# Kernel tuning notes

Hardware: AMD Instinct MI355X
Metric: run time of the kernel (lower is better)

The kernel has to match this reference:

```python
import jax, jax.numpy as jnp
import numpy as np

N, E = 16384, 262144
NS_N, NV_N = 128, 64      # node irreps: 128x0e + 64x1o
NS_E, NV_E = 64, 32       # edge irreps: 64x0e + 32x1o
C_OH, LAT = 16, 128
DS, DV = 128, 64          # irreps_out: 128x0e + 64x1o
GS = DS + DV              # gate input scalars (128 act scalars + 64 gates)
SC = 2 * NS_N + NS_E      # 320 concatenated scalar channels
VC = 2 * NV_N + NV_E      # 160 concatenated l=1 channels
M0_IN = SC + VC           # 480 m=0 features into SO2 linear
M0_OUT = GS + DV          # 256 m=0 outputs
AVG_NEI = 16.0
EPS = 1e-8


def setup_inputs() -> dict:
    key = jax.random.key(0)
    ks = jax.random.split(key, 20)
    f = lambda k, s: jax.random.normal(k, s, dtype=jnp.float32)
    return dict(
        node_feat=f(ks[0], (N, NS_N + 3 * NV_N)),
        edge_feat=f(ks[1], (E, NS_E + 3 * NV_E)),
        edge_vec=f(ks[2], (E, 3)),
        latents=f(ks[3], (E, LAT)),
        node_onehot=jax.nn.one_hot(jax.random.randint(ks[4], (N,), 0, C_OH), C_OH, dtype=jnp.float32),
        ln_n_g0=jnp.ones(NS_N), ln_n_b0=jnp.zeros(NS_N), ln_n_g1=jnp.ones(NV_N),
        ln_e_g0=jnp.ones(NS_E), ln_e_b0=jnp.zeros(NS_E), ln_e_g1=jnp.ones(NV_E),
        W_m0=f(ks[5], (M0_IN, M0_OUT)),
        w_r=f(ks[6], (VC, DV)), w_i=f(ks[7], (VC, DV)),
        W_env=f(ks[8], (LAT, DS + DV)),
        Wp0=f(ks[9], (DS, DS)), bp0=jnp.zeros(DS), Wpv=f(ks[10], (DV, DV)),
        Wtp0=f(ks[11], (DS, C_OH, GS)), Wtp1=f(ks[12], (DV, C_OH, DV)),
        Wo0=f(ks[13], (DS, DS)), bo0=jnp.zeros(DS), Wov=f(ks[14], (DV, DV)),
        res_param=jnp.zeros(()),
        edge_index=jax.random.randint(ks[15], (2, E), 0, N),
    )


def _sep_ln(s, v, g0, b0, g1):
    # separable equivariant layer norm: LN on scalars, per-sample RMS on l=1 block
    mu = s.mean(-1, keepdims=True)
    var = jnp.mean((s - mu) ** 2, -1, keepdims=True)
    s = (s - mu) * jax.lax.rsqrt(var + EPS) * g0 + b0
    vvar = jnp.mean(v * v, axis=(-2, -1), keepdims=True)  # component norm, degree-balanced (single l=1)
    v = v * jax.lax.rsqrt(vvar + EPS) * g1[None, :, None]
    return s, v


def _edge_frame(vec):
    # orthonormal frame (a, e1, e2) with a along the edge
    a = vec * jax.lax.rsqrt(jnp.sum(vec * vec, -1, keepdims=True) + EPS)
    helper = jnp.where(jnp.abs(a[:, 2:3]) < 0.99,
                       jnp.array([0.0, 0.0, 1.0], dtype=vec.dtype),
                       jnp.array([1.0, 0.0, 0.0], dtype=vec.dtype))
    e1 = jnp.cross(helper, a)
    e1 = e1 * jax.lax.rsqrt(jnp.sum(e1 * e1, -1, keepdims=True) + EPS)
    e2 = jnp.cross(a, e1)
    return a, e1, e2


def reference(node_feat, edge_feat, edge_vec, latents, node_onehot,
              ln_n_g0, ln_n_b0, ln_n_g1, ln_e_g0, ln_e_b0, ln_e_g1,
              W_m0, w_r, w_i, W_env, Wp0, bp0, Wpv,
              Wtp0, Wtp1, Wo0, bo0, Wov, res_param, edge_index):
    src, dst = edge_index[0], edge_index[1]
    ns, nv = node_feat[:, :NS_N], node_feat[:, NS_N:].reshape(-1, NV_N, 3)
    es, ev = edge_feat[:, :NS_E], edge_feat[:, NS_E:].reshape(-1, NV_E, 3)
    ns, nv = _sep_ln(ns, nv, ln_n_g0, ln_n_b0, ln_n_g1)
    es, ev = _sep_ln(es, ev, ln_e_g0, ln_e_b0, ln_e_g1)
    # per-edge concat: node[src] + edge + node[dst]
    s_cat = jnp.concatenate([ns[src], es, ns[dst]], -1)          # [E, SC]
    v_cat = jnp.concatenate([nv[src], ev, nv[dst]], 1)           # [E, VC, 3]
    # SO2 linear: rotate into edge frame, mix per |m|, rotate back
    a, e1, e2 = _edge_frame(edge_vec)
    c0 = jnp.einsum('eci,ei->ec', v_cat, a)
    c1 = jnp.einsum('eci,ei->ec', v_cat, e1)
    c2 = jnp.einsum('eci,ei->ec', v_cat, e2)
    m0 = jnp.concatenate([s_cat, c0], -1) @ W_m0 * (1.0 / np.sqrt(M0_IN))  # [E, M0_OUT]
    s_out, c0o = m0[:, :GS], m0[:, GS:]
    inv = 1.0 / np.sqrt(VC)
    c1o = (c1 @ w_r - c2 @ w_i) * inv
    c2o = (c1 @ w_i + c2 @ w_r) * inv
    v_out = (c0o[..., None] * a[:, None, :] + c1o[..., None] * e1[:, None, :]
             + c2o[..., None] * e2[:, None, :])                  # [E, DV, 3]
    # gate activation
    s_act = jax.nn.silu(s_out[:, :DS])
    gates = jax.nn.sigmoid(s_out[:, DS:])
    v_g = v_out * gates[..., None]
    # lin_post (per-l linear, scalar bias)
    s2 = s_act @ Wp0 * (1.0 / np.sqrt(DS)) + bp0
    v2 = jnp.einsum('eui,uv->evi', v_g, Wpv) * (1.0 / np.sqrt(DV))
    # env weighting from latents (E3ElementLinear, per-irrep-channel scalars)
    w = latents @ W_env * (1.0 / np.sqrt(LAT))
    s2 = s2 * w[:, :DS]
    v2 = v2 * w[:, DS:, None]
    nrm = 1.0 / np.sqrt(AVG_NEI)
    sa = jax.ops.segment_sum(s2, dst, num_segments=N) * nrm
    va = jax.ops.segment_sum(v2, dst, num_segments=N) * nrm
    # one-hot FullyConnectedTensorProduct (in2 all 0e) + gate + linear
    t0 = jnp.einsum('nu,nc,ucv->nv', sa, node_onehot, Wtp0) * (1.0 / np.sqrt(DS * C_OH))
    t1 = jnp.einsum('nui,nc,ucv->nvi', va, node_onehot, Wtp1) * (1.0 / np.sqrt(DV * C_OH))
    s3 = jax.nn.silu(t0[:, :DS])
    v3 = t1 * jax.nn.sigmoid(t0[:, DS:])[..., None]
    s4 = s3 @ Wo0 * (1.0 / np.sqrt(DS)) + bo0
    v4 = jnp.einsum('nui,uv->nvi', v3, Wov) * (1.0 / np.sqrt(DV))
    new = jnp.concatenate([s4, v4.reshape(-1, 3 * DV)], -1)
    r = jax.nn.sigmoid(res_param)
    return r * node_feat + (1.0 - r) * new
```

## Files before the change

### kernel.cpp

```cpp
#include <hip/hip_runtime.h>
#include <math.h>

#define N_NODES 16384
#define N_EDGES 262144
#define EPSF 1e-8f

#define OFF_X     0
#define OFF_C12   31232
#define OFF_FR    52224
#define OFF_EDST  53760
#define POOL_BYTES 53888
#define OFF_SACT  0
#define OFF_GATE  8704
#define OFF_C0O   17408
#define OFF_C1O   31232
#define OFF_C2O   39936
#define OFF_VG    8704

typedef __bf16 bf16x8 __attribute__((ext_vector_type(8)));
typedef float  f32x4  __attribute__((ext_vector_type(4)));

__device__ __forceinline__ f32x4 MFMA16(bf16x8 a, bf16x8 b, f32x4 c){
  return __builtin_amdgcn_mfma_f32_16x16x32_bf16(a, b, c, 0, 0, 0);
}

__device__ __forceinline__ unsigned short f2bf(float x){
  union { float f; unsigned u; } c; c.f = x;
  unsigned u = c.u;
  u += 0x7FFFu + ((u>>16)&1u);
  return (unsigned short)(u>>16);
}
__device__ __forceinline__ float bf2f(unsigned short h){
  union { unsigned u; float f; } c; c.u = ((unsigned)h)<<16;
  return c.f;
}
__device__ __forceinline__ float wsum64(float v){
  #pragma unroll
  for (int m=1; m<64; m<<=1) v += __shfl_xor(v, m);
  return v;
}
__device__ __forceinline__ float wsum32(float v){
  #pragma unroll
  for (int m=1; m<32; m<<=1) v += __shfl_xor(v, m);
  return v;
}
__device__ __forceinline__ float sigm(float x){ return 1.0f/(1.0f+__expf(-x)); }
__device__ __forceinline__ float silu(float x){ return x/(1.0f+__expf(-x)); }

__global__ __launch_bounds__(256) void k_pack(const float* __restrict__ src,
                                              unsigned short* __restrict__ dst,
                                              int K, int N){
  int i = blockIdx.x*256 + threadIdx.x;
  if (i >= K*N) return;
  int k = i / N, n = i - k*N;
  int idx = (((k>>5)*N + n)*4 + ((k>>3)&3))*8 + (k&7);
  dst[idx] = f2bf(src[i]);
}
__global__ __launch_bounds__(256) void k_pack_wc(const float* __restrict__ wr,
                                                 const float* __restrict__ wi,
                                                 unsigned short* __restrict__ dst){
  int i = blockIdx.x*256 + threadIdx.x;
  if (i >= 320*128) return;
  int k = i >> 7, n = i & 127;
  float v;
  if (k < 160) v = (n < 64) ? wr[k*64 + n]        : wi[k*64 + (n-64)];
  else         v = (n < 64) ? -wi[(k-160)*64 + n] : wr[(k-160)*64 + (n-64)];
  int idx = (((k>>5)*128 + n)*4 + ((k>>3)&3))*8 + (k&7);
  dst[idx] = f2bf(v);
}

__global__ __launch_bounds__(256) void k_hist(const int* __restrict__ eidx, int* __restrict__ cnt){
  int e = blockIdx.x*256 + threadIdx.x;
  if (e < N_EDGES) atomicAdd(&cnt[eidx[N_EDGES+e]], 1);
}
__global__ __launch_bounds__(256) void k_scan(const int* __restrict__ cnt,
                                              int* __restrict__ rowp, int* __restrict__ cursor){
  __shared__ int part[256];
  __shared__ int pref[257];
  const int t = threadIdx.x;
  const int base = t*64;
  int s = 0;
  for (int i=0;i<64;i++) s += cnt[base+i];
  part[t] = s; __syncthreads();
  if (t==0){ int a=0; for (int i=0;i<256;i++){ pref[i]=a; a+=part[i]; } pref[256]=a; }
  __syncthreads();
  int a = pref[t];
  for (int i=0;i<64;i++){ rowp[base+i]=a; cursor[base+i]=a; a += cnt[base+i]; }
  if (t==0) rowp[N_NODES] = pref[256];
}
__global__ __launch_bounds__(256) void k_fill(const int* __restrict__ eidx,
                                              int* __restrict__ cursor, int* __restrict__ perm){
  int e = blockIdx.x*256 + threadIdx.x;
  if (e < N_EDGES){
    int pos = atomicAdd(&cursor[eidx[N_EDGES+e]], 1);
    perm[pos] = e;
  }
}

__global__ __launch_bounds__(256) void k_node_ln(
    const float* __restrict__ nf, const float* __restrict__ g0,
    const float* __restrict__ b0, const float* __restrict__ g1,
    unsigned short* __restrict__ ns_ln, float* __restrict__ nv_ln)
{
  const int tid  = threadIdx.x;
  const int lane = tid & 63;
  const int n    = blockIdx.x*4 + (tid>>6);
  const float* row = nf + (size_t)n*320;

  float s0 = row[lane], s1 = row[64+lane];
  float mu = wsum64(s0+s1) * (1.0f/128.0f);
  float d0 = s0-mu, d1 = s1-mu;
  float var = wsum64(d0*d0+d1*d1) * (1.0f/128.0f);
  float rs = rsqrtf(var + EPSF);
  ns_ln[(size_t)n*128 + lane]    = f2bf(d0*rs*g0[lane]    + b0[lane]);
  ns_ln[(size_t)n*128 + 64+lane] = f2bf(d1*rs*g0[64+lane] + b0[64+lane]);

  float px = row[128+lane*3+0], py = row[128+lane*3+1], pz = row[128+lane*3+2];
  float vvar = wsum64(px*px+py*py+pz*pz) * (1.0f/192.0f);
  float vsc = rsqrtf(vvar + EPSF) * g1[lane];
  nv_ln[(size_t)n*192 + lane*3+0] = px*vsc;
  nv_ln[(size_t)n*192 + lane*3+1] = py*vsc;
  nv_ln[(size_t)n*192 + lane*3+2] = pz*vsc;
}

__global__ __launch_bounds__(256) void k_wenv(
  const float* __restrict__ lats, const unsigned short* __restrict__ pWenv,
  const int* __restrict__ perm, unsigned short* __restrict__ wbuf)
{
  __shared__ unsigned short A[64*136];
  const int tid = threadIdx.x;
  {
    const int row = tid>>2, part = tid&3;
    const int slot = blockIdx.x*64 + row;
    const int e = perm[slot];
    const float* lr = lats + (size_t)e*128 + part*32;
    #pragma unroll
    for (int q=0;q<8;q++){
      float4 v = *(const float4*)(lr + q*4);
      int cb = part*32 + q*4;
      A[row*136 + cb+0] = f2bf(v.x);
      A[row*136 + cb+1] = f2bf(v.y);
      A[row*136 + cb+2] = f2bf(v.z);
      A[row*136 + cb+3] = f2bf(v.w);
    }
  }
  __syncthreads();
  const int wid = tid>>6, l = tid&63, r15 = l&15, g = l>>4;
  const f32x4 zero4 = {0.f,0.f,0.f,0.f};
  f32x4 acc[4][3];
  #pragma unroll
  for (int m=0;m<4;m++)
    #pragma unroll
    for (int n=0;n<3;n++) acc[m][n]=zero4;

  const unsigned short* bbase = pWenv + ((size_t)(wid*48 + r15)*4 + g)*8;
  #pragma unroll
  for (int kc=0;kc<4;kc++){
    bf16x8 b[3];
    #pragma unroll
    for (int n=0;n<3;n++) b[n] = *(const bf16x8*)(bbase + (size_t)kc*6144 + n*512);
    #pragma unroll
    for (int m=0;m<4;m++){
      bf16x8 a = *(const bf16x8*)&A[(m*16+r15)*136 + kc*32 + g*8];
      #pragma unroll
      for (int n=0;n<3;n++) acc[m][n] = MFMA16(a, b[n], acc[m][n]);
    }
  }
  #pragma unroll
  for (int m=0;m<4;m++)
    #pragma unroll
    for (int n=0;n<3;n++)
      #pragma unroll
      for (int r=0;r<4;r++){
        int sr = m*16 + g*4 + r;
        int j  = wid*48 + n*16 + r15;
        wbuf[(size_t)(blockIdx.x*64 + sr)*192 + j] = f2bf(acc[m][n][r]*0.08838834764831845f);
      }
}

__global__ __launch_bounds__(256,3) void k_edge(
  const float* __restrict__ ef, const float* __restrict__ evec,
  const float* __restrict__ g0e, const float* __restrict__ b0e, const float* __restrict__ g1e,
  const unsigned short* __restrict__ pWm0, const unsigned short* __restrict__ pWc,
  const unsigned short* __restrict__ pWp0, const unsigned short* __restrict__ pWpv,
  const float* __restrict__ bp0,
  const int* __restrict__ eidx, const int* __restrict__ perm,
  const unsigned short* __restrict__ ns_ln, const float* __restrict__ nv_ln,
  const unsigned short* __restrict__ wbuf,
  float* __restrict__ sa, float* __restrict__ va)
{
  extern __shared__ unsigned char pool[];
  const int tid = threadIdx.x;
  unsigned short* Xs   = (unsigned short*)(pool + OFF_X);
  unsigned short* C12s = (unsigned short*)(pool + OFF_C12);
  float* FRf = (float*)(pool + OFF_FR);
  int*   EDST = (int*)(pool + OFF_EDST);

  {
    const int ln = tid & 31;
    #pragma unroll
    for (int eo=0; eo<4; ++eo){
      const int el = eo*8 + (tid>>5);
      const int slot = blockIdx.x*32 + el;
      const size_t e = (size_t)perm[slot];
      const int src = eidx[e];
      const int dst = eidx[N_EDGES + e];

      float vx=evec[e*3+0], vy=evec[e*3+1], vz=evec[e*3+2];
      float rn = rsqrtf(vx*vx+vy*vy+vz*vz+EPSF);
      float ax=vx*rn, ay=vy*rn, az=vz*rn;
      float hx, hz;
      if (fabsf(az) < 0.99f){ hx=0.f; hz=1.f; } else { hx=1.f; hz=0.f; }
      float e1x = -hz*ay;
      float e1y = hz*ax - hx*az;
      float e1z = hx*ay;
      float rn1 = rsqrtf(e1x*e1x+e1y*e1y+e1z*e1z+EPSF);
      e1x*=rn1; e1y*=rn1; e1z*=rn1;
      float e2x = ay*e1z - az*e1y;
      float e2y = az*e1x - ax*e1z;
      float e2z = ax*e1y - ay*e1x;
      if (ln==0){
        FRf[el*12+0]=ax;  FRf[el*12+1]=ay;  FRf[el*12+2]=az;
        FRf[el*12+3]=e1x; FRf[el*12+4]=e1y; FRf[el*12+5]=e1z;
        FRf[el*12+6]=e2x; FRf[el*12+7]=e2y; FRf[el*12+8]=e2z;
        EDST[el]=dst;
      }

      const float* erow = ef + e*160;
      float s0=erow[ln], s1=erow[32+ln];
      float mu = wsum32(s0+s1)*(1.f/64.f);
      float d0=s0-mu, d1=s1-mu;
      float var = wsum32(d0*d0+d1*d1)*(1.f/64.f);
      float rs = rsqrtf(var+EPSF);
      Xs[el*488 + 128+ln] = f2bf(d0*rs*g0e[ln]    + b0e[ln]);
      Xs[el*488 + 160+ln] = f2bf(d1*rs*g0e[32+ln] + b0e[32+ln]);

      float wx=erow[64+ln*3+0], wy=erow[64+ln*3+1], wz=erow[64+ln*3+2];
      float vvar = wsum32(wx*wx+wy*wy+wz*wz)*(1.f/96.f);
      float vsc = rsqrtf(vvar+EPSF)*g1e[ln];
      wx*=vsc; wy*=vsc; wz*=vsc;
      Xs  [el*488 + 320+64+ln]   = f2bf(wx*ax +wy*ay +wz*az);
      C12s[el*328 + 64+ln]       = f2bf(wx*e1x+wy*e1y+wz*e1z);
      C12s[el*328 + 160+64+ln]   = f2bf(wx*e2x+wy*e2y+wz*e2z);

      const unsigned short* nss = ns_ln + (size_t)src*128;
      const unsigned short* nsd = ns_ln + (size_t)dst*128;
      *(uint2*)&Xs[el*488 + ln*4]       = *(const uint2*)&nss[ln*4];
      *(uint2*)&Xs[el*488 + 192 + ln*4] = *(const uint2*)&nsd[ln*4];

      const float* nvs = nv_ln + (size_t)src*192;
      const float* nvd = nv_ln + (size_t)dst*192;
      #pragma unroll
      for (int q=0;q<2;q++){
        int u = ln+32*q;
        float px=nvs[u*3+0], py=nvs[u*3+1], pz=nvs[u*3+2];
        Xs  [el*488 + 320+u]     = f2bf(px*ax +py*ay +pz*az);
        C12s[el*328 + u]         = f2bf(px*e1x+py*e1y+pz*e1z);
        C12s[el*328 + 160+u]     = f2bf(px*e2x+py*e2y+pz*e2z);
        px=nvd[u*3+0]; py=nvd[u*3+1]; pz=nvd[u*3+2];
        Xs  [el*488 + 320+96+u]  = f2bf(px*ax +py*ay +pz*az);
        C12s[el*328 + 96+u]      = f2bf(px*e1x+py*e1y+pz*e1z);
        C12s[el*328 + 160+96+u]  = f2bf(px*e2x+py*e2y+pz*e2z);
      }
    }
  }
  __syncthreads();

  const int wid = tid>>6, l = tid&63;
  const int r15 = l&15, g = l>>4;
  const f32x4 zero4 = {0.f,0.f,0.f,0.f};

  f32x4 acc1[2][4], acc2[2][2];
  #pragma unroll
  for (int m=0;m<2;m++){
    #pragma unroll
    for (int n=0;n<4;n++) acc1[m][n]=zero4;
    #pragma unroll
    for (int n=0;n<2;n++) acc2[m][n]=zero4;
  }

  {
    const unsigned short* bbase = pWm0 + ((size_t)(wid*64 + r15)*4 + g)*8;
    bf16x8 bc[4];
    #pragma unroll
    for (int n=0;n<4;n++) bc[n] = *(const bf16x8*)(bbase + n*512);
    for (int kc=0;kc<15;kc++){
      bf16x8 a0 = *(const bf16x8*)&Xs[(    r15)*488 + kc*32 + g*8];
      bf16x8 a1 = *(const bf16x8*)&Xs[(16+ r15)*488 + kc*32 + g*8];
      bf16x8 bn[4];
      if (kc<14){
        const unsigned short* np = bbase + (size_t)(kc+1)*8192;
        #pragma unroll
        for (int n=0;n<4;n++) bn[n] = *(const bf16x8*)(np + n*512);
      }
      #pragma unroll
      for (int n=0;n<4;n++){
        acc1[0][n] = MFMA16(a0,bc[n],acc1[0][n]);
        acc1[1][n] = MFMA16(a1,bc[n],acc1[1][n]);
      }
      #pragma unroll
      for (int n=0;n<4;n++) bc[n]=bn[n];
    }
  }
  {
    const unsigned short* bbase = pWc + ((size_t)(wid*32 + r15)*4 + g)*8;
    bf16x8 bc[2];
    #pragma unroll
    for (int n=0;n<2;n++) bc[n] = *(const bf16x8*)(bbase + n*512);
    for (int kc=0;kc<10;kc++){
      bf16x8 a0 = *(const bf16x8*)&C12s[(    r15)*328 + kc*32 + g*8];
      bf16x8 a1 = *(const bf16x8*)&C12s[(16+ r15)*328 + kc*32 + g*8];
      bf16x8 bn[2];
      if (kc<9){
        const unsigned short* np = bbase + (size_t)(kc+1)*4096;
        #pragma unroll
        for (int n=0;n<2;n++) bn[n] = *(const bf16x8*)(np + n*512);
      }
      #pragma unroll
      for (int n=0;n<2;n++){
        acc2[0][n] = MFMA16(a0,bc[n],acc2[0][n]);
        acc2[1][n] = MFMA16(a1,bc[n],acc2[1][n]);
      }
      #pragma unroll
      for (int n=0;n<2;n++) bc[n]=bn[n];
    }
  }

  __syncthreads();

  {
    unsigned short* SAs = (unsigned short*)(pool + OFF_SACT);
    float* GAf = (float*)(pool + OFF_GATE);
    float* C0f = (float*)(pool + OFF_C0O);
    #pragma unroll
    for (int m=0;m<2;m++)
      #pragma unroll
      for (int n=0;n<4;n++)
        #pragma unroll
        for (int r=0;r<4;r++){
          int e = m*16 + g*4 + r;
          int j = wid*64 + n*16 + r15;
          float v = acc1[m][n][r]*0.04564354645876384f;
          if (j < 128)      SAs[e*136 + j] = f2bf(silu(v));
          else if (j < 192) GAf[e*68 + (j-128)] = sigm(v);
          else              C0f[e*68 + (j-192)] = v;
        }
    float* C1f = (float*)(pool + OFF_C1O);
    float* C2f = (float*)(pool + OFF_C2O);
    #pragma unroll
    for (int m=0;m<2;m++)
      #pragma unroll
      for (int n=0;n<2;n++)
        #pragma unroll
        for (int r=0;r<4;r++){
          int e = m*16 + g*4 + r;
          int j = wid*32 + n*16 + r15;
          float v = acc2[m][n][r]*0.07905694150420949f;
          if (j < 64) C1f[e*68 + j] = v;
          else        C2f[e*68 + (j-64)] = v;
        }
  }
  __syncthreads();

  {
    const int e = tid>>3, u0 = (tid&7)*8;
    const float* GAf = (const float*)(pool + OFF_GATE);
    const float* C0f = (const float*)(pool + OFF_C0O);
    const float* C1f = (const float*)(pool + OFF_C1O);
    const float* C2f = (const float*)(pool + OFF_C2O);
    float ax=FRf[e*12+0],  ay=FRf[e*12+1],  az=FRf[e*12+2];
    float b1x=FRf[e*12+3], b1y=FRf[e*12+4], b1z=FRf[e*12+5];
    float b2x=FRf[e*12+6], b2y=FRf[e*12+7], b2z=FRf[e*12+8];
    float vgx[8], vgy[8], vgz[8];
    #pragma unroll
    for (int i=0;i<8;i++){
      int u = u0+i;
      float gt = GAf[e*68+u];
      float c0 = C0f[e*68+u], c1 = C1f[e*68+u], c2 = C2f[e*68+u];
      vgx[i] = (c0*ax + c1*b1x + c2*b2x)*gt;
      vgy[i] = (c0*ay + c1*b1y + c2*b2y)*gt;
      vgz[i] = (c0*az + c1*b1z + c2*b2z)*gt;
    }
    __syncthreads();
    unsigned short* VGs = (unsigned short*)(pool + OFF_VG);
    #pragma unroll
    for (int i=0;i<8;i++){
      VGs[0*2304 + e*72 + u0+i] = f2bf(vgx[i]);
      VGs[1*2304 + e*72 + u0+i] = f2bf(vgy[i]);
      VGs[2*2304 + e*72 + u0+i] = f2bf(vgz[i]);
    }
  }
  __syncthreads();

  {
    const unsigned short* SAs = (const unsigned short*)(pool + OFF_SACT);
    const unsigned short* VGs = (const unsigned short*)(pool + OFF_VG);
    const int sbase = blockIdx.x*32;

    float wsc[2][2][4], wvc[2][4], bp0v[2];
    #pragma unroll
    for (int n=0;n<2;n++) bp0v[n] = bp0[wid*32 + n*16 + r15];
    #pragma unroll
    for (int m=0;m<2;m++)
      #pragma unroll
      for (int r=0;r<4;r++){
        int e = m*16 + g*4 + r;
        #pragma unroll
        for (int n=0;n<2;n++)
          wsc[m][n][r] = bf2f(wbuf[(size_t)(sbase+e)*192 + wid*32 + n*16 + r15]);
        wvc[m][r] = bf2f(wbuf[(size_t)(sbase+e)*192 + 128 + wid*16 + r15]);
      }

    f32x4 acc4[2][2], acc5[3][2];
    #pragma unroll
    for (int m=0;m<2;m++){ acc4[m][0]=zero4; acc4[m][1]=zero4; }
    #pragma unroll
    for (int c=0;c<3;c++){ acc5[c][0]=zero4; acc5[c][1]=zero4; }

    {
      const unsigned short* bbase = pWp0 + ((size_t)(wid*32 + r15)*4 + g)*8;
      #pragma unroll
      for (int kc=0;kc<4;kc++){
        bf16x8 a0 = *(const bf16x8*)&SAs[(    r15)*136 + kc*32 + g*8];
        bf16x8 a1 = *(const bf16x8*)&SAs[(16+ r15)*136 + kc*32 + g*8];
        #pragma unroll
        for (int n=0;n<2;n++){
          bf16x8 b = *(const bf16x8*)(bbase + (size_t)kc*4096 + n*512);
          acc4[0][n] = MFMA16(a0,b,acc4[0][n]);
          acc4[1][n] = MFMA16(a1,b,acc4[1][n]);
        }
      }
    }
    {
      bf16x8 b5[2];
      #pragma unroll
      for (int kc=0;kc<2;kc++)
        b5[kc] = *(const bf16x8*)(pWpv + ((size_t)(kc*64 + wid*16 + r15)*4 + g)*8);
      #pragma unroll
      for (int c=0;c<3;c++)
        #pragma unroll
        for (int kc=0;kc<2;kc++){
          bf16x8 a0 = *(const bf16x8*)&VGs[c*2304 + (    r15)*72 + kc*32 + g*8];
          bf16x8 a1 = *(const bf16x8*)&VGs[c*2304 + (16+ r15)*72 + kc*32 + g*8];
          acc5[c][0] = MFMA16(a0,b5[kc],acc5[c][0]);
          acc5[c][1] = MFMA16(a1,b5[kc],acc5[c][1]);
        }
    }

    __syncthreads();
    float* R = (float*)pool;
    #pragma unroll
    for (int m=0;m<2;m++)
      #pragma unroll
      for (int n=0;n<2;n++)
        #pragma unroll
        for (int r=0;r<4;r++){
          int e = m*16 + g*4 + r;
          int j = wid*32 + n*16 + r15;
          R[e*320 + j] = (acc4[m][n][r]*0.08838834764831845f + bp0v[n]) * wsc[m][n][r];
        }
    #pragma unroll
    for (int c=0;c<3;c++)
      #pragma unroll
      for (int m=0;m<2;m++)
        #pragma unroll
        for (int r=0;r<4;r++){
          int e = m*16 + g*4 + r;
          int vch = wid*16 + r15;
          R[e*320 + 128 + vch*3 + c] = acc5[c][m][r]*0.125f * wvc[m][r];
        }
    __syncthreads();

    for (int j = tid; j < 320; j += 256){
      float accv = R[j];
      int cur = EDST[0];
      for (int e=1;e<32;e++){
        int d = EDST[e];
        float v = R[e*320 + j];
        if (d != cur){
          float* tgt = (j<128) ? &sa[(size_t)cur*128 + j] : &va[(size_t)cur*192 + (j-128)];
          atomicAdd(tgt, accv);
          accv = v; cur = d;
        } else accv += v;
      }
      float* tgt = (j<128) ? &sa[(size_t)cur*128 + j] : &va[(size_t)cur*192 + (j-128)];
      atomicAdd(tgt, accv);
    }
  }
}

__global__ __launch_bounds__(256) void k_node_out(
  const float* __restrict__ nf, const float* __restrict__ oh,
  const float* __restrict__ Wtp0, const float* __restrict__ Wtp1,
  const float* __restrict__ Wo0, const float* __restrict__ bo0,
  const float* __restrict__ Wov, const float* __restrict__ resp,
  const float* __restrict__ sa, const float* __restrict__ va,
  float* __restrict__ out)
{
  __shared__ float SAB[4][128];
  __shared__ float VX[4][64], VY[4][64], VZ[4][64];
  __shared__ float S3 [4][128];
  __shared__ float V3 [4][256];
  const int tid=threadIdx.x, lane=tid&63, g=tid>>6;
  const int n = blockIdx.x*4 + g;

  float cf=0.f;
  #pragma unroll
  for (int j=0;j<16;j++) cf += j*oh[(size_t)n*16+j];
  const int c = (int)(cf+0.5f);

  SAB[g][lane]    = sa[(size_t)n*128+lane]   *0.25f;
  SAB[g][64+lane] = sa[(size_t)n*128+64+lane]*0.25f;
  VX[g][lane] = va[(size_t)n*192+lane*3+0]*0.25f;
  VY[g][lane] = va[(size_t)n*192+lane*3+1]*0.25f;
  VZ[g][lane] = va[(size_t)n*192+lane*3+2]*0.25f;
  __syncthreads();

  float t00=0.f, t01=0.f, t02=0.f;
  const float* w0c = Wtp0 + (size_t)c*192;
  for (int u=0;u<128;u++){
    float s = SAB[g][u];
    t00 += s * w0c[(size_t)u*3072 + lane];
    t01 += s * w0c[(size_t)u*3072 + lane+64];
    t02 += s * w0c[(size_t)u*3072 + lane+128];
  }
  const float sct0 = 0.02209708691f;
  t00*=sct0; t01*=sct0; t02*=sct0;

  float t1x=0.f,t1y=0.f,t1z=0.f;
  const float* w1c = Wtp1 + (size_t)c*64;
  for (int u=0;u<64;u++){
    float wv = w1c[(size_t)u*1024 + lane];
    t1x += VX[g][u]*wv;
    t1y += VY[g][u]*wv;
    t1z += VZ[g][u]*wv;
  }
  t1x*=0.03125f; t1y*=0.03125f; t1z*=0.03125f;

  S3[g][lane]    = silu(t00);
  S3[g][64+lane] = silu(t01);
  float g2 = sigm(t02);
  float4 v3v = {t1x*g2, t1y*g2, t1z*g2, 0.f};
  *(float4*)&V3[g][lane*4] = v3v;
  __syncthreads();

  float s40=0.f, s41=0.f;
  for (int k=0;k<128;k++){
    float s3k = S3[g][k];
    s40 += s3k*Wo0[k*128+lane];
    s41 += s3k*Wo0[k*128+64+lane];
  }
  s40 = s40*0.08838834765f + bo0[lane];
  s41 = s41*0.08838834765f + bo0[64+lane];

  float v4x=0.f,v4y=0.f,v4z=0.f;
  for (int u=0;u<64;u++){
    float4 v3u = *(const float4*)&V3[g][u*4];
    float wv = Wov[u*64+lane];
    v4x += v3u.x*wv; v4y += v3u.y*wv; v4z += v3u.z*wv;
  }
  v4x*=0.125f; v4y*=0.125f; v4z*=0.125f;

  const float r = sigm(resp[0]);
  const float* row = nf + (size_t)n*320;
  float* orow = out + (size_t)n*320;
  orow[lane]      = r*row[lane]      + (1.f-r)*s40;
  orow[64+lane]   = r*row[64+lane]   + (1.f-r)*s41;
  orow[128+lane*3+0] = r*row[128+lane*3+0] + (1.f-r)*v4x;
  orow[128+lane*3+1] = r*row[128+lane*3+1] + (1.f-r)*v4y;
  orow[128+lane*3+2] = r*row[128+lane*3+2] + (1.f-r)*v4z;
}

extern "C" void kernel_launch(void* const* d_in, const int* in_sizes, int n_in,
                              void* d_out, int out_size, void* d_ws, size_t ws_size,
                              hipStream_t stream)
{
  const float* nf   = (const float*)d_in[0];
  const float* ef   = (const float*)d_in[1];
  const float* evec = (const float*)d_in[2];
  const float* lats = (const float*)d_in[3];
  const float* oh   = (const float*)d_in[4];
  const float* g0n  = (const float*)d_in[5];
  const float* b0n  = (const float*)d_in[6];
  const float* g1n  = (const float*)d_in[7];
  const float* g0e  = (const float*)d_in[8];
  const float* b0e  = (const float*)d_in[9];
  const float* g1e  = (const float*)d_in[10];
  const float* Wm0  = (const float*)d_in[11];
  const float* wr   = (const float*)d_in[12];
  const float* wi   = (const float*)d_in[13];
  const float* Wenv = (const float*)d_in[14];
  const float* Wp0  = (const float*)d_in[15];
  const float* bp0  = (const float*)d_in[16];
  const float* Wpv  = (const float*)d_in[17];
  const float* Wtp0 = (const float*)d_in[18];
  const float* Wtp1 = (const float*)d_in[19];
  const float* Wo0  = (const float*)d_in[20];
  const float* bo0  = (const float*)d_in[21];
  const float* Wov  = (const float*)d_in[22];
  const float* resp = (const float*)d_in[23];
  const int*   eidx = (const int*)d_in[24];

  char* base = (char*)d_ws;
  unsigned short* ns_ln = (unsigned short*)(base);
  float* nv_ln = (float*)(base + 4194304);
  float* sa    = (float*)(base + 16777216);
  float* va    = (float*)(base + 25165824);
  unsigned short* wpk = (unsigned short*)(base + 37748736);
  unsigned short* pWm0  = wpk;
  unsigned short* pWc   = wpk + 122880;
  unsigned short* pWenv = wpk + 163840;
  unsigned short* pWp0  = wpk + 188416;
  unsigned short* pWpv  = wpk + 204800;
  int* ibuf   = (int*)(base + 38166528);
  int* cnt    = ibuf;
  int* rowp   = ibuf + 16384;
  int* cursor = ibuf + 32769;
  int* perm   = ibuf + 49153;
  unsigned short* wbuf = (unsigned short*)(base + 39411720);

  hipMemsetAsync(sa, 0, (size_t)N_NODES*320*sizeof(float), stream);
  hipMemsetAsync(cnt, 0, N_NODES*sizeof(int), stream);

  k_pack<<<(122880+255)/256, 256, 0, stream>>>(Wm0,  pWm0, 480, 256);
  k_pack_wc<<<(40960+255)/256, 256, 0, stream>>>(wr, wi, pWc);
  k_pack<<<(24576+255)/256, 256, 0, stream>>>(Wenv, pWenv, 128, 192);
  k_pack<<<(16384+255)/256, 256, 0, stream>>>(Wp0,  pWp0, 128, 128);
  k_pack<<<(4096+255)/256,  256, 0, stream>>>(Wpv,  pWpv, 64, 64);
  k_node_ln<<<N_NODES/4, 256, 0, stream>>>(nf, g0n, b0n, g1n, ns_ln, nv_ln);

  k_hist<<<(N_EDGES+255)/256, 256, 0, stream>>>(eidx, cnt);
  k_scan<<<1, 256, 0, stream>>>(cnt, rowp, cursor);
  k_fill<<<(N_EDGES+255)/256, 256, 0, stream>>>(eidx, cursor, perm);

  k_wenv<<<N_EDGES/64, 256, 0, stream>>>(lats, pWenv, perm, wbuf);

  k_edge<<<N_EDGES/32, 256, POOL_BYTES, stream>>>(ef, evec, g0e, b0e, g1e,
                                                  pWm0, pWc, pWp0, pWpv, bp0,
                                                  eidx, perm, ns_ln, nv_ln, wbuf,
                                                  sa, va);
  k_node_out<<<N_NODES/4, 256, 0, stream>>>(nf, oh, Wtp0, Wtp1, Wo0, bo0, Wov,
                                            resp, sa, va, (float*)d_out);
}
```

Measured before the change: 686.1 us.

## Store node vectors and edge frames in fp16, fuse weight packing kernels

Node l=1 layer-norm output and the per-edge frame in shared memory switch from fp32 to fp16, halving gather traffic for neighbor vectors and shrinking the LDS pool. The five weight-pack launches become one kernel, and bf16 conversion uses the native cast. The env-weight loads from wbuf are hoisted to the start of the edge kernel so their latency overlaps the gather phase. Together these cut memory traffic and launch count, at the cost of fp16 rounding on vector features and frames and higher register pressure from values held across the kernel.

```diff
diff --git a/kernel.cpp b/kernel.cpp
--- a/kernel.cpp
+++ b/kernel.cpp
@@ -8,8 +8,8 @@
 #define OFF_X     0
 #define OFF_C12   31232
 #define OFF_FR    52224
-#define OFF_EDST  53760
-#define POOL_BYTES 53888
+#define OFF_EDST  52992
+#define POOL_BYTES 53120
 #define OFF_SACT  0
 #define OFF_GATE  8704
 #define OFF_C0O   17408
@@ -25,10 +25,9 @@
 }
 
 __device__ __forceinline__ unsigned short f2bf(float x){
-  union { float f; unsigned u; } c; c.f = x;
-  unsigned u = c.u;
-  u += 0x7FFFu + ((u>>16)&1u);
-  return (unsigned short)(u>>16);
+  __bf16 h = (__bf16)x;
+  union { __bf16 b; unsigned short u; } c; c.b = h;
+  return c.u;
 }
 __device__ __forceinline__ float bf2f(unsigned short h){
   union { unsigned u; float f; } c; c.u = ((unsigned)h)<<16;
@@ -47,26 +46,41 @@
 __device__ __forceinline__ float sigm(float x){ return 1.0f/(1.0f+__expf(-x)); }
 __device__ __forceinline__ float silu(float x){ return x/(1.0f+__expf(-x)); }
 
-__global__ __launch_bounds__(256) void k_pack(const float* __restrict__ src,
-                                              unsigned short* __restrict__ dst,
-                                              int K, int N){
+__global__ __launch_bounds__(256) void k_pack_all(
+  const float* __restrict__ Wm0, const float* __restrict__ wr,
+  const float* __restrict__ wi,  const float* __restrict__ Wenv,
+  const float* __restrict__ Wp0, const float* __restrict__ Wpv,
+  unsigned short* __restrict__ wpk)
+{
   int i = blockIdx.x*256 + threadIdx.x;
-  if (i >= K*N) return;
-  int k = i / N, n = i - k*N;
-  int idx = (((k>>5)*N + n)*4 + ((k>>3)&3))*8 + (k&7);
-  dst[idx] = f2bf(src[i]);
-}
-__global__ __launch_bounds__(256) void k_pack_wc(const float* __restrict__ wr,
-                                                 const float* __restrict__ wi,
-                                                 unsigned short* __restrict__ dst){
-  int i = blockIdx.x*256 + threadIdx.x;
-  if (i >= 320*128) return;
-  int k = i >> 7, n = i & 127;
-  float v;
-  if (k < 160) v = (n < 64) ? wr[k*64 + n]        : wi[k*64 + (n-64)];
-  else         v = (n < 64) ? -wi[(k-160)*64 + n] : wr[(k-160)*64 + (n-64)];
-  int idx = (((k>>5)*128 + n)*4 + ((k>>3)&3))*8 + (k&7);
-  dst[idx] = f2bf(v);
+  if (i < 122880){
+    int k = i >> 8, n = i & 255;
+    int idx = (((k>>5)*256 + n)*4 + ((k>>3)&3))*8 + (k&7);
+    wpk[idx] = f2bf(Wm0[i]);
+  } else if (i < 163840){
+    int j = i - 122880;
+    int k = j >> 7, n = j & 127;
+    float v;
+    if (k < 160) v = (n < 64) ? wr[k*64 + n]        : wi[k*64 + (n-64)];
+    else         v = (n < 64) ? -wi[(k-160)*64 + n] : wr[(k-160)*64 + (n-64)];
+    int idx = (((k>>5)*128 + n)*4 + ((k>>3)&3))*8 + (k&7);
+    wpk[122880 + idx] = f2bf(v);
+  } else if (i < 188416){
+    int j = i - 163840;
+    int k = j / 192, n = j - k*192;
+    int idx = (((k>>5)*192 + n)*4 + ((k>>3)&3))*8 + (k&7);
+    wpk[163840 + idx] = f2bf(Wenv[j]);
+  } else if (i < 204800){
+    int j = i - 188416;
+    int k = j >> 7, n = j & 127;
+    int idx = (((k>>5)*128 + n)*4 + ((k>>3)&3))*8 + (k&7);
+    wpk[188416 + idx] = f2bf(Wp0[j]);
+  } else if (i < 208896){
+    int j = i - 204800;
+    int k = j >> 6, n = j & 63;
+    int idx = (((k>>5)*64 + n)*4 + ((k>>3)&3))*8 + (k&7);
+    wpk[204800 + idx] = f2bf(Wpv[j]);
+  }
 }
 
 __global__ __launch_bounds__(256) void k_hist(const int* __restrict__ eidx, int* __restrict__ cnt){
@@ -100,7 +114,7 @@
 __global__ __launch_bounds__(256) void k_node_ln(
     const float* __restrict__ nf, const float* __restrict__ g0,
     const float* __restrict__ b0, const float* __restrict__ g1,
-    unsigned short* __restrict__ ns_ln, float* __restrict__ nv_ln)
+    unsigned short* __restrict__ ns_ln, _Float16* __restrict__ nv_ln)
 {
   const int tid  = threadIdx.x;
   const int lane = tid & 63;
@@ -118,9 +132,9 @@
   float px = row[128+lane*3+0], py = row[128+lane*3+1], pz = row[128+lane*3+2];
   float vvar = wsum64(px*px+py*py+pz*pz) * (1.0f/192.0f);
   float vsc = rsqrtf(vvar + EPSF) * g1[lane];
-  nv_ln[(size_t)n*192 + lane*3+0] = px*vsc;
-  nv_ln[(size_t)n*192 + lane*3+1] = py*vsc;
-  nv_ln[(size_t)n*192 + lane*3+2] = pz*vsc;
+  nv_ln[(size_t)n*192 + lane*3+0] = (_Float16)(px*vsc);
+  nv_ln[(size_t)n*192 + lane*3+1] = (_Float16)(py*vsc);
+  nv_ln[(size_t)n*192 + lane*3+2] = (_Float16)(pz*vsc);
 }
 
 __global__ __launch_bounds__(256) void k_wenv(
@@ -185,7 +199,7 @@
   const unsigned short* __restrict__ pWp0, const unsigned short* __restrict__ pWpv,
   const float* __restrict__ bp0,
   const int* __restrict__ eidx, const int* __restrict__ perm,
-  const unsigned short* __restrict__ ns_ln, const float* __restrict__ nv_ln,
+  const unsigned short* __restrict__ ns_ln, const _Float16* __restrict__ nv_ln,
   const unsigned short* __restrict__ wbuf,
   float* __restrict__ sa, float* __restrict__ va)
 {
@@ -193,8 +207,26 @@
   const int tid = threadIdx.x;
   unsigned short* Xs   = (unsigned short*)(pool + OFF_X);
   unsigned short* C12s = (unsigned short*)(pool + OFF_C12);
-  float* FRf = (float*)(pool + OFF_FR);
+  _Float16* FRh = (_Float16*)(pool + OFF_FR);
   int*   EDST = (int*)(pool + OFF_EDST);
+
+  const int wid = tid>>6, l = tid&63;
+  const int r15 = l&15, g = l>>4;
+
+  const int sbase = blockIdx.x*32;
+  float wsc[2][2][4], wvc[2][4], bp0v[2];
+  #pragma unroll
+  for (int n=0;n<2;n++) bp0v[n] = bp0[wid*32 + n*16 + r15];
+  #pragma unroll
+  for (int m=0;m<2;m++)
+    #pragma unroll
+    for (int r=0;r<4;r++){
+      int e = m*16 + g*4 + r;
+      #pragma unroll
+      for (int n=0;n<2;n++)
+        wsc[m][n][r] = bf2f(wbuf[(size_t)(sbase+e)*192 + wid*32 + n*16 + r15]);
+      wvc[m][r] = bf2f(wbuf[(size_t)(sbase+e)*192 + 128 + wid*16 + r15]);
+    }
 
   {
     const int ln = tid & 31;
@@ -220,9 +252,9 @@
       float e2y = az*e1x - ax*e1z;
       float e2z = ax*e1y - ay*e1x;
       if (ln==0){
-        FRf[el*12+0]=ax;  FRf[el*12+1]=ay;  FRf[el*12+2]=az;
-        FRf[el*12+3]=e1x; FRf[el*12+4]=e1y; FRf[el*12+5]=e1z;
-        FRf[el*12+6]=e2x; FRf[el*12+7]=e2y; FRf[el*12+8]=e2z;
+        FRh[el*12+0]=(_Float16)ax;  FRh[el*12+1]=(_Float16)ay;  FRh[el*12+2]=(_Float16)az;
+        FRh[el*12+3]=(_Float16)e1x; FRh[el*12+4]=(_Float16)e1y; FRh[el*12+5]=(_Float16)e1z;
+        FRh[el*12+6]=(_Float16)e2x; FRh[el*12+7]=(_Float16)e2y; FRh[el*12+8]=(_Float16)e2z;
         EDST[el]=dst;
       }
 
@@ -248,16 +280,16 @@
       *(uint2*)&Xs[el*488 + ln*4]       = *(const uint2*)&nss[ln*4];
       *(uint2*)&Xs[el*488 + 192 + ln*4] = *(const uint2*)&nsd[ln*4];
 
-      const float* nvs = nv_ln + (size_t)src*192;
-      const float* nvd = nv_ln + (size_t)dst*192;
+      const _Float16* nvs = nv_ln + (size_t)src*192;
+      const _Float16* nvd = nv_ln + (size_t)dst*192;
       #pragma unroll
       for (int q=0;q<2;q++){
         int u = ln+32*q;
-        float px=nvs[u*3+0], py=nvs[u*3+1], pz=nvs[u*3+2];
+        float px=(float)nvs[u*3+0], py=(float)nvs[u*3+1], pz=(float)nvs[u*3+2];
         Xs  [el*488 + 320+u]     = f2bf(px*ax +py*ay +pz*az);
         C12s[el*328 + u]         = f2bf(px*e1x+py*e1y+pz*e1z);
         C12s[el*328 + 160+u]     = f2bf(px*e2x+py*e2y+pz*e2z);
-        px=nvd[u*3+0]; py=nvd[u*3+1]; pz=nvd[u*3+2];
+        px=(float)nvd[u*3+0]; py=(float)nvd[u*3+1]; pz=(float)nvd[u*3+2];
         Xs  [el*488 + 320+96+u]  = f2bf(px*ax +py*ay +pz*az);
         C12s[el*328 + 96+u]      = f2bf(px*e1x+py*e1y+pz*e1z);
         C12s[el*328 + 160+96+u]  = f2bf(px*e2x+py*e2y+pz*e2z);
@@ -266,8 +298,6 @@
   }
   __syncthreads();
 
-  const int wid = tid>>6, l = tid&63;
-  const int r15 = l&15, g = l>>4;
   const f32x4 zero4 = {0.f,0.f,0.f,0.f};
 
   f32x4 acc1[2][4], acc2[2][2];
@@ -368,9 +398,9 @@
     const float* C0f = (const float*)(pool + OFF_C0O);
     const float* C1f = (const float*)(pool + OFF_C1O);
     const float* C2f = (const float*)(pool + OFF_C2O);
-    float ax=FRf[e*12+0],  ay=FRf[e*12+1],  az=FRf[e*12+2];
-    float b1x=FRf[e*12+3], b1y=FRf[e*12+4], b1z=FRf[e*12+5];
-    float b2x=FRf[e*12+6], b2y=FRf[e*12+7], b2z=FRf[e*12+8];
+    float ax=(float)FRh[e*12+0],  ay=(float)FRh[e*12+1],  az=(float)FRh[e*12+2];
+    float b1x=(float)FRh[e*12+3], b1y=(float)FRh[e*12+4], b1z=(float)FRh[e*12+5];
+    float b2x=(float)FRh[e*12+6], b2y=(float)FRh[e*12+7], b2z=(float)FRh[e*12+8];
     float vgx[8], vgy[8], vgz[8];
     #pragma unroll
     for (int i=0;i<8;i++){
@@ -395,21 +425,6 @@
   {
     const unsigned short* SAs = (const unsigned short*)(pool + OFF_SACT);
     const unsigned short* VGs = (const unsigned short*)(pool + OFF_VG);
-    const int sbase = blockIdx.x*32;
-
-    float wsc[2][2][4], wvc[2][4], bp0v[2];
-    #pragma unroll
-    for (int n=0;n<2;n++) bp0v[n] = bp0[wid*32 + n*16 + r15];
-    #pragma unroll
-    for (int m=0;m<2;m++)
-      #pragma unroll
-      for (int r=0;r<4;r++){
-        int e = m*16 + g*4 + r;
-        #pragma unroll
-        for (int n=0;n<2;n++)
-          wsc[m][n][r] = bf2f(wbuf[(size_t)(sbase+e)*192 + wid*32 + n*16 + r15]);
-        wvc[m][r] = bf2f(wbuf[(size_t)(sbase+e)*192 + 128 + wid*16 + r15]);
-      }
 
     f32x4 acc4[2][2], acc5[3][2];
     #pragma unroll
@@ -603,30 +618,26 @@
 
   char* base = (char*)d_ws;
   unsigned short* ns_ln = (unsigned short*)(base);
-  float* nv_ln = (float*)(base + 4194304);
-  float* sa    = (float*)(base + 16777216);
-  float* va    = (float*)(base + 25165824);
-  unsigned short* wpk = (unsigned short*)(base + 37748736);
+  _Float16* nv_ln = (_Float16*)(base + 4194304);
+  float* sa    = (float*)(base + 10485760);
+  float* va    = (float*)(base + 18874368);
+  unsigned short* wpk = (unsigned short*)(base + 31457280);
   unsigned short* pWm0  = wpk;
   unsigned short* pWc   = wpk + 122880;
   unsigned short* pWenv = wpk + 163840;
   unsigned short* pWp0  = wpk + 188416;
   unsigned short* pWpv  = wpk + 204800;
-  int* ibuf   = (int*)(base + 38166528);
+  int* ibuf   = (int*)(base + 31875072);
   int* cnt    = ibuf;
   int* rowp   = ibuf + 16384;
   int* cursor = ibuf + 32769;
   int* perm   = ibuf + 49153;
-  unsigned short* wbuf = (unsigned short*)(base + 39411720);
+  unsigned short* wbuf = (unsigned short*)(base + 33120264);
 
   hipMemsetAsync(sa, 0, (size_t)N_NODES*320*sizeof(float), stream);
   hipMemsetAsync(cnt, 0, N_NODES*sizeof(int), stream);
 
-  k_pack<<<(122880+255)/256, 256, 0, stream>>>(Wm0,  pWm0, 480, 256);
-  k_pack_wc<<<(40960+255)/256, 256, 0, stream>>>(wr, wi, pWc);
-  k_pack<<<(24576+255)/256, 256, 0, stream>>>(Wenv, pWenv, 128, 192);
-  k_pack<<<(16384+255)/256, 256, 0, stream>>>(Wp0,  pWp0, 128, 128);
-  k_pack<<<(4096+255)/256,  256, 0, stream>>>(Wpv,  pWpv, 64, 64);
+  k_pack_all<<<(208896+255)/256, 256, 0, stream>>>(Wm0, wr, wi, Wenv, Wp0, Wpv, wpk);
   k_node_ln<<<N_NODES/4, 256, 0, stream>>>(nf, g0n, b0n, g1n, ns_ln, nv_ln);
 
   k_hist<<<(N_EDGES+255)/256, 256, 0, stream>>>(eidx, cnt);
```

New measurement: 591.2 us. 13.8% less time.
